# Kernel tuning notes

Hardware: AMD Instinct MI355X
Metric: run time of the kernel (lower is better)

Reference implementation:

```python
import jax, jax.numpy as jnp
import numpy as np

N_NODES = 50000
N_EDGES = 800000
NUM_GRAPHS = 256
F_IN = 64        # num_features (per-head out dim == in dim in this module)
HEADS = 4        # n_heads1
OUT_DIM = 128    # output_dim
HC = HEADS * F_IN
NEG_SLOPE = 0.2  # GATConv leaky_relu slope
EPS = 1e-5       # GraphNorm eps


def setup_inputs() -> dict:
    key = jax.random.key(0)
    ks = jax.random.split(key, 12)
    s = lambda k, shape, fan: (jax.random.normal(k, shape, jnp.float32) / np.sqrt(fan).astype(np.float32))
    return {
        "x": jax.random.normal(ks[0], (N_NODES, F_IN), jnp.float32),
        "edge_index": jax.random.randint(ks[1], (2, N_EDGES), 0, N_NODES),
        "batch": jnp.sort(jax.random.randint(ks[2], (N_NODES,), 0, NUM_GRAPHS)),
        # GATConv params
        "lin_w": s(ks[3], (HC, F_IN), F_IN),
        "att_src": s(ks[4], (HEADS, F_IN), F_IN),
        "att_dst": s(ks[5], (HEADS, F_IN), F_IN),
        "gat_bias": jnp.zeros((HC,), jnp.float32),
        # GraphNorm params
        "gn_weight": jnp.ones((HC,), jnp.float32),
        "gn_bias": jnp.zeros((HC,), jnp.float32),
        "gn_mean_scale": jnp.ones((HC,), jnp.float32),
        # fc_g1 / out heads
        "fc1_w": s(ks[6], (OUT_DIM, HC), HC), "fc1_b": jnp.zeros((OUT_DIM,), jnp.float32),
        "out_w": s(ks[7], (1, OUT_DIM), OUT_DIM), "out_b": jnp.zeros((1,), jnp.float32),
        # GlobalAttention gate_nn: Linear(HC,16) -> ReLU -> Linear(16,1) -> Sigmoid
        "att1_w": s(ks[8], (16, HC), HC), "att1_b": jnp.zeros((16,), jnp.float32),
        "att2_w": s(ks[9], (1, 16), 16), "att2_b": jnp.zeros((1,), jnp.float32),
    }


def _gat_conv(x, edge_index, lin_w, att_src, att_dst, gat_bias):
    """PyG GATConv with add_self_loops=True, concat heads. Returns (out [N,HC], alpha [E+N,H])."""
    N = x.shape[0]
    xh = (x @ lin_w.T).reshape(N, HEADS, F_IN)                 # [N,H,C]
    a_src = (xh * att_src[None]).sum(-1)                        # [N,H]
    a_dst = (xh * att_dst[None]).sum(-1)                        # [N,H]
    loops = jnp.arange(N)
    src = jnp.concatenate([edge_index[0], loops])               # [E+N]
    dst = jnp.concatenate([edge_index[1], loops])
    alpha = jax.nn.leaky_relu(a_src[src] + a_dst[dst], NEG_SLOPE)  # [E+N,H]
    # segment softmax over incoming edges of each dst node (self-loops guarantee non-empty)
    amax = jax.ops.segment_max(alpha, dst, num_segments=N)
    alpha = jnp.exp(alpha - amax[dst])
    denom = jax.ops.segment_sum(alpha, dst, num_segments=N)
    alpha = alpha / (denom[dst] + 1e-16)
    msg = xh[src] * alpha[:, :, None]                           # [E+N,H,C]
    out = jax.ops.segment_sum(msg, dst, num_segments=N).reshape(N, HC) + gat_bias
    return out, alpha


def _graph_norm(x, batch, weight, bias, mean_scale):
    ones = jnp.ones((x.shape[0],), x.dtype)
    cnt = jnp.maximum(jax.ops.segment_sum(ones, batch, num_segments=NUM_GRAPHS), 1.0)[:, None]
    mean = jax.ops.segment_sum(x, batch, num_segments=NUM_GRAPHS) / cnt
    sub = x - mean[batch] * mean_scale
    var = jax.ops.segment_sum(sub * sub, batch, num_segments=NUM_GRAPHS) / cnt
    return weight * sub / jnp.sqrt(var + EPS)[batch] + bias


def _global_attention(x, batch, att1_w, att1_b, att2_w, att2_b):
    gate = jax.nn.sigmoid(jax.nn.relu(x @ att1_w.T + att1_b) @ att2_w.T + att2_b)  # [N,1]
    gmax = jax.ops.segment_max(gate, batch, num_segments=NUM_GRAPHS)
    gate = jnp.exp(gate - gmax[batch])
    gden = jax.ops.segment_sum(gate, batch, num_segments=NUM_GRAPHS)
    gate = gate / (gden[batch] + 1e-16)
    return jax.ops.segment_sum(gate * x, batch, num_segments=NUM_GRAPHS)  # [G,HC]


def reference(x, edge_index, batch, lin_w, att_src, att_dst, gat_bias,
              gn_weight, gn_bias, gn_mean_scale, fc1_w, fc1_b, out_w, out_b,
              att1_w, att1_b, att2_w, att2_b):
    x2, alpha = _gat_conv(x, edge_index, lin_w, att_src, att_dst, gat_bias)
    h = _graph_norm(x2, batch, gn_weight, gn_bias, gn_mean_scale)
    h = jax.nn.relu(h)                                # node_dropout = identity (eval)
    pooled = _global_attention(h, batch, att1_w, att1_b, att2_w, att2_b)
    h = jax.nn.relu(pooled @ fc1_w.T + fc1_b)          # dropout = identity (eval)
    out = jax.nn.sigmoid(h @ out_w.T + out_b)          # [G,1]
    return out, alpha
```

## Files before the change

### kernel.cpp

```cpp
#include <hip/hip_runtime.h>
#include <hip/hip_fp16.h>
#include <math.h>

#define NN 50000
#define NE 800000
#define NG 256
#define NEG_SLOPE 0.2f
#define GEPS 1e-5f
#define NB 196
#define CAP 6144
#define EPB 3125
#define SPLIT 8
#define NLINB 782
#define ABLK 3321

typedef _Float16 f16x8 __attribute__((ext_vector_type(8)));
typedef _Float16 f16x4 __attribute__((ext_vector_type(4)));
typedef float f32x4 __attribute__((ext_vector_type(4)));
typedef float f32x2 __attribute__((ext_vector_type(2)));

__device__ __forceinline__ float lrelu(float v){ return v > 0.f ? v : NEG_SLOPE * v; }

__global__ __launch_bounds__(256) void k_misc(const float* __restrict__ lin_w,
                                              _Float16* __restrict__ wh,
                                              const float* __restrict__ att1_w,
                                              _Float16* __restrict__ a1w,
                                              const int* __restrict__ batch,
                                              int* __restrict__ goff,
                                              int* __restrict__ gcnt,
                                              int* __restrict__ bucket_cnt) {
  int b = blockIdx.x, tid = threadIdx.x;
  if (b == 0) {
    if (tid < NB) bucket_cnt[tid] = 0;
    int g = tid;
    int lo = 0, hi = NN;
    while (lo < hi) { int mid = (lo + hi) >> 1; if (batch[mid] < g) lo = mid + 1; else hi = mid; }
    int start = lo;
    lo = 0; hi = NN;
    while (lo < hi) { int mid = (lo + hi) >> 1; if (batch[mid] < g + 1) lo = mid + 1; else hi = mid; }
    goff[g] = start;
    gcnt[g] = lo - start;
  } else if (b <= 16) {
    int i0 = (b - 1) * 1024 + tid * 4;
    float4 f = *(const float4*)&lin_w[i0];
    f16x4 h4;
    h4[0] = (_Float16)f.x; h4[1] = (_Float16)f.y; h4[2] = (_Float16)f.z; h4[3] = (_Float16)f.w;
    *(f16x4*)&wh[i0] = h4;
  } else {
    int i0 = (b - 17) * 1024 + tid * 4;
    float4 f = *(const float4*)&att1_w[i0];
    f16x4 h4;
    h4[0] = (_Float16)f.x; h4[1] = (_Float16)f.y; h4[2] = (_Float16)f.z; h4[3] = (_Float16)f.w;
    *(f16x4*)&a1w[i0] = h4;
  }
}

__device__ __forceinline__ void lin_body(char* smem,
                                         const float* __restrict__ x,
                                         const _Float16* __restrict__ wh,
                                         const float* __restrict__ att_src,
                                         const float* __restrict__ att_dst,
                                         unsigned char* __restrict__ xh8,
                                         float* __restrict__ a_src_n,
                                         float* __restrict__ a_dst_n) {
  unsigned char* s_f8 = (unsigned char*)smem;
  int w = threadIdx.x >> 6, lane = threadIdx.x & 63;
  int nb = blockIdx.x * 64 + w * 16;
  if (nb >= NN) return;
  int am = lane & 15, quad = lane >> 4;
  int wb = w * 4096;

  const float* xr = x + (size_t)(nb + am) * 64 + quad * 8;
  float4 f0 = *(const float4*)(xr);
  float4 f1 = *(const float4*)(xr + 4);
  float4 f2 = *(const float4*)(xr + 32);
  float4 f3 = *(const float4*)(xr + 36);
  f16x8 a0, a1;
  a0[0] = (_Float16)f0.x; a0[1] = (_Float16)f0.y; a0[2] = (_Float16)f0.z; a0[3] = (_Float16)f0.w;
  a0[4] = (_Float16)f1.x; a0[5] = (_Float16)f1.y; a0[6] = (_Float16)f1.z; a0[7] = (_Float16)f1.w;
  a1[0] = (_Float16)f2.x; a1[1] = (_Float16)f2.y; a1[2] = (_Float16)f2.z; a1[3] = (_Float16)f2.w;
  a1[4] = (_Float16)f3.x; a1[5] = (_Float16)f3.y; a1[6] = (_Float16)f3.z; a1[7] = (_Float16)f3.w;

  f32x4 acc[16];
#pragma unroll
  for (int ct = 0; ct < 16; ct++) acc[ct] = (f32x4){0.f, 0.f, 0.f, 0.f};

#pragma unroll
  for (int ct = 0; ct < 16; ct++) {
    const _Float16* wbp = wh + (size_t)(ct * 16 + am) * 64 + quad * 8;
    f16x8 b0 = *(const f16x8*)(wbp);
    f16x8 b1 = *(const f16x8*)(wbp + 32);
    acc[ct] = __builtin_amdgcn_mfma_f32_16x16x32_f16(a0, b0, acc[ct], 0, 0, 0);
    acc[ct] = __builtin_amdgcn_mfma_f32_16x16x32_f16(a1, b1, acc[ct], 0, 0, 0);
  }

  float ps[4][4], pd[4][4];
#pragma unroll
  for (int r = 0; r < 4; r++)
#pragma unroll
    for (int h = 0; h < 4; h++) { ps[r][h] = 0.f; pd[r][h] = 0.f; }
#pragma unroll
  for (int ct = 0; ct < 16; ct++) {
    int c = ct * 16 + am;
    float av = att_src[c];
    float dv = att_dst[c];
    int h = ct >> 2;
#pragma unroll
    for (int r = 0; r < 4; r++) {
      float v = acc[ct][r];
      ps[r][h] += v * av;
      pd[r][h] += v * dv;
    }
  }
#pragma unroll
  for (int r = 0; r < 4; r++)
#pragma unroll
    for (int h = 0; h < 4; h++) {
      float s = ps[r][h], d = pd[r][h];
#pragma unroll
      for (int o = 1; o < 16; o <<= 1) {
        s += __shfl_xor(s, o, 64);
        d += __shfl_xor(d, o, 64);
      }
      if (am == 0) {
        int node = nb + quad * 4 + r;
        a_src_n[node * 4 + h] = s;
        a_dst_n[node * 4 + h] = d;
      }
    }

#pragma unroll
  for (int r = 0; r < 4; r++) {
    uint4 u;
    int t;
    t = __builtin_amdgcn_cvt_pk_fp8_f32(acc[0][r],  acc[1][r],  0, 0);
    t = __builtin_amdgcn_cvt_pk_fp8_f32(acc[2][r],  acc[3][r],  t, 1);
    u.x = (unsigned)t;
    t = __builtin_amdgcn_cvt_pk_fp8_f32(acc[4][r],  acc[5][r],  0, 0);
    t = __builtin_amdgcn_cvt_pk_fp8_f32(acc[6][r],  acc[7][r],  t, 1);
    u.y = (unsigned)t;
    t = __builtin_amdgcn_cvt_pk_fp8_f32(acc[8][r],  acc[9][r],  0, 0);
    t = __builtin_amdgcn_cvt_pk_fp8_f32(acc[10][r], acc[11][r], t, 1);
    u.z = (unsigned)t;
    t = __builtin_amdgcn_cvt_pk_fp8_f32(acc[12][r], acc[13][r], 0, 0);
    t = __builtin_amdgcn_cvt_pk_fp8_f32(acc[14][r], acc[15][r], t, 1);
    u.w = (unsigned)t;
    *(uint4*)&s_f8[wb + (quad * 4 + r) * 256 + am * 16] = u;
  }
#pragma unroll
  for (int p = 0; p < 4; p++) {
    uint4 u = *(const uint4*)&s_f8[wb + p * 1024 + lane * 16];
    *(uint4*)&xh8[(size_t)nb * 256 + p * 1024 + lane * 16] = u;
  }
}

__device__ __forceinline__ void binA_body(char* smem, int b,
                                          const int* __restrict__ ei,
                                          int* __restrict__ bucket_cnt,
                                          int2* __restrict__ ebuf) {
  int2* sorted = (int2*)smem;
  int*  hist   = (int*)(smem + 25024);
  int*  lbase  = (int*)(smem + 25824);
  int*  cur    = (int*)(smem + 26624);
  int*  runb   = (int*)(smem + 27424);
  int*  wsum   = (int*)(smem + 28224);
  int tid = threadIdx.x, lane = tid & 63, wid = tid >> 6;
  int e0 = b * EPB, e1 = min(e0 + EPB, NE);
  int n = e1 - e0;
  for (int i = tid; i < NB; i += 256) hist[i] = 0;
  __syncthreads();
  for (int e = e0 + tid; e < e1; e += 256) atomicAdd(&hist[ei[NE + e] >> 8], 1);
  __syncthreads();
  {
    int v = (tid < NB) ? hist[tid] : 0;
    int s = v;
#pragma unroll
    for (int o = 1; o < 64; o <<= 1) { int t = __shfl_up(s, o, 64); if (lane >= o) s += t; }
    if (lane == 63) wsum[wid] = s;
    __syncthreads();
    int wbase = 0;
    for (int k = 0; k < wid; k++) wbase += wsum[k];
    if (tid < NB) {
      int ex = wbase + s - v;
      lbase[tid] = ex;
      cur[tid] = ex;
      runb[tid] = atomicAdd(&bucket_cnt[tid], v);
    }
  }
  __syncthreads();
  for (int e = e0 + tid; e < e1; e += 256) {
    int d = ei[NE + e], s = ei[e];
    int lp = atomicAdd(&cur[d >> 8], 1);
    sorted[lp] = make_int2(d, s);
  }
  __syncthreads();
  for (int i = tid; i < n; i += 256) {
    int2 e = sorted[i];
    int bk = e.x >> 8;
    int slot = runb[bk] + (i - lbase[bk]);
    if (slot < CAP) ebuf[(size_t)bk * CAP + slot] = e;
  }
}

__global__ __launch_bounds__(256) void k_linbin(const float* __restrict__ x,
                                                const _Float16* __restrict__ wh,
                                                const float* __restrict__ att_src,
                                                const float* __restrict__ att_dst,
                                                unsigned char* __restrict__ xh8,
                                                float* __restrict__ a_src_n,
                                                float* __restrict__ a_dst_n,
                                                const int* __restrict__ ei,
                                                int* __restrict__ bucket_cnt,
                                                int2* __restrict__ ebuf) {
  __shared__ __align__(16) char smem[28240];
  if (blockIdx.x < NLINB)
    lin_body(smem, x, wh, att_src, att_dst, xh8, a_src_n, a_dst_n);
  else
    binA_body(smem, blockIdx.x - NLINB, ei, bucket_cnt, ebuf);
}

__global__ __launch_bounds__(256) void k_binB(const int2* __restrict__ ebuf,
                                              const int* __restrict__ bucket_cnt,
                                              int* __restrict__ deg,
                                              int* __restrict__ offs,
                                              int* __restrict__ src_list) {
  __shared__ int hist[256];
  __shared__ int cur[256];
  __shared__ int wsum[4];
  __shared__ int bbase[NB];
  int b = blockIdx.x, tid = threadIdx.x, lane = tid & 63, wid = tid >> 6;
  {
    int v = (tid < NB) ? min(bucket_cnt[tid], CAP) : 0;
    int s = v;
#pragma unroll
    for (int o = 1; o < 64; o <<= 1) { int t = __shfl_up(s, o, 64); if (lane >= o) s += t; }
    if (lane == 63) wsum[wid] = s;
    __syncthreads();
    int wbase = 0;
    for (int k = 0; k < wid; k++) wbase += wsum[k];
    if (tid < NB) bbase[tid] = wbase + s - v;
  }
  __syncthreads();
  int cnt = min(bucket_cnt[b], CAP);
  int base = bbase[b];
  const int2* seg = ebuf + (size_t)b * CAP;
  hist[tid] = 0;
  __syncthreads();
  for (int i = tid; i < cnt; i += 256) atomicAdd(&hist[seg[i].x & 255], 1);
  __syncthreads();
  int v = hist[tid];
  int s = v;
#pragma unroll
  for (int o = 1; o < 64; o <<= 1) { int t = __shfl_up(s, o, 64); if (lane >= o) s += t; }
  if (lane == 63) wsum[wid] = s;
  __syncthreads();
  int wbase = 0;
  for (int k = 0; k < wid; k++) wbase += wsum[k];
  int excl = wbase + s - v;
  int node = b * 256 + tid;
  if (node < NN) {
    deg[node] = v;
    offs[node] = base + excl;
  }
  cur[tid] = excl;
  __syncthreads();
  for (int i = tid; i < cnt; i += 256) {
    int2 e = seg[i];
    int pos = base + atomicAdd(&cur[e.x & 255], 1);
    src_list[pos] = e.y;
  }
}

__global__ __launch_bounds__(64) void k_gat(const unsigned char* __restrict__ xh8,
                                            const float* __restrict__ a_src_n,
                                            const float* __restrict__ a_dst_n,
                                            const int* __restrict__ offs,
                                            const int* __restrict__ deg_arr,
                                            const int* __restrict__ src_list,
                                            const float* __restrict__ gat_bias,
                                            __half* __restrict__ x2h,
                                            float* __restrict__ den_inv) {
  __shared__ __align__(16) float s_al[64 * 4];
  __shared__ int s_src[64];
  __shared__ __half s_tr[256];
  int n = blockIdx.x, lane = threadIdx.x;
  int off = offs[n], dg = deg_arr[n], cnt = dg + 1;
  float4 ad = *(const float4*)&a_dst_n[n * 4];
  int am = lane & 15, eg = lane >> 4;
  unsigned loff = (unsigned)am * 16u;

  f32x4 acc[4];
#pragma unroll
  for (int w = 0; w < 4; w++) acc[w] = (f32x4){0.f, 0.f, 0.f, 0.f};
  float s0 = 0.f, s1 = 0.f, s2 = 0.f, s3 = 0.f;

  for (int cb = 0; cb < cnt; cb += 64) {
    int clen = min(64, cnt - cb);
    int pad = (clen + 3) & ~3;
    if (lane < clen) {
      int j = cb + lane;
      int src = (j < dg) ? src_list[off + j] : n;
      float4 as = *(const float4*)&a_src_n[src * 4];
      float e0 = __expf(lrelu(as.x + ad.x));
      float e1 = __expf(lrelu(as.y + ad.y));
      float e2 = __expf(lrelu(as.z + ad.z));
      float e3 = __expf(lrelu(as.w + ad.w));
      s_src[lane] = src;
      *(float4*)&s_al[lane * 4] = make_float4(e0, e1, e2, e3);
      s0 += e0; s1 += e1; s2 += e2; s3 += e3;
    } else if (lane < pad) {
      s_src[lane] = n;
      *(float4*)&s_al[lane * 4] = make_float4(0.f, 0.f, 0.f, 0.f);
    }
    __syncthreads();
    for (int j = 0; j < pad; j += 4) {
      int e = j + eg;
      unsigned oA = ((unsigned)s_src[e] << 8) + loff;
      uint4 r = *(const uint4*)&xh8[oA];
      float4 a4 = *(const float4*)&s_al[e * 4];
      f32x2 l0 = __builtin_amdgcn_cvt_pk_f32_fp8((int)r.x, 0);
      f32x2 h0 = __builtin_amdgcn_cvt_pk_f32_fp8((int)r.x, 1);
      f32x2 l1 = __builtin_amdgcn_cvt_pk_f32_fp8((int)r.y, 0);
      f32x2 h1 = __builtin_amdgcn_cvt_pk_f32_fp8((int)r.y, 1);
      f32x2 l2 = __builtin_amdgcn_cvt_pk_f32_fp8((int)r.z, 0);
      f32x2 h2 = __builtin_amdgcn_cvt_pk_f32_fp8((int)r.z, 1);
      f32x2 l3 = __builtin_amdgcn_cvt_pk_f32_fp8((int)r.w, 0);
      f32x2 h3 = __builtin_amdgcn_cvt_pk_f32_fp8((int)r.w, 1);
      acc[0][0] += a4.x * l0[0]; acc[0][1] += a4.x * l0[1];
      acc[0][2] += a4.x * h0[0]; acc[0][3] += a4.x * h0[1];
      acc[1][0] += a4.y * l1[0]; acc[1][1] += a4.y * l1[1];
      acc[1][2] += a4.y * h1[0]; acc[1][3] += a4.y * h1[1];
      acc[2][0] += a4.z * l2[0]; acc[2][1] += a4.z * l2[1];
      acc[2][2] += a4.z * h2[0]; acc[2][3] += a4.z * h2[1];
      acc[3][0] += a4.w * l3[0]; acc[3][1] += a4.w * l3[1];
      acc[3][2] += a4.w * h3[0]; acc[3][3] += a4.w * h3[1];
    }
    __syncthreads();
  }

#pragma unroll
  for (int o = 32; o >= 1; o >>= 1) {
    s0 += __shfl_xor(s0, o, 64);
    s1 += __shfl_xor(s1, o, 64);
    s2 += __shfl_xor(s2, o, 64);
    s3 += __shfl_xor(s3, o, 64);
  }
  float i0 = 1.f / (s0 + 1e-16f), i1 = 1.f / (s1 + 1e-16f);
  float i2 = 1.f / (s2 + 1e-16f), i3 = 1.f / (s3 + 1e-16f);
  if (lane == 0) *(float4*)&den_inv[n * 4] = make_float4(i0, i1, i2, i3);

#pragma unroll
  for (int w = 0; w < 4; w++)
#pragma unroll
    for (int k = 0; k < 4; k++) {
      float v = acc[w][k];
      v += __shfl_xor(v, 16, 64);
      v += __shfl_xor(v, 32, 64);
      acc[w][k] = v;
    }

  float ivw = (eg == 0) ? i0 : (eg == 1) ? i1 : (eg == 2) ? i2 : i3;
#pragma unroll
  for (int k = 0; k < 4; k++) {
    int c = (4 * eg + k) * 16 + am;
    s_tr[c] = __float2half(acc[eg][k] * ivw + gat_bias[c]);
  }
  __syncthreads();
  uint2 u = *(const uint2*)&s_tr[4 * lane];
  *(uint2*)&x2h[(size_t)n * 256 + 4 * lane] = u;
}

__global__ __launch_bounds__(256) void k_alst(const int* __restrict__ ei,
                                              const float* __restrict__ a_src_n,
                                              const float* __restrict__ a_dst_n,
                                              const float* __restrict__ den_inv,
                                              float* __restrict__ alpha_out,
                                              const __half* __restrict__ x2h,
                                              const int* __restrict__ gcnt,
                                              const int* __restrict__ goff,
                                              float* __restrict__ psumA,
                                              float* __restrict__ psumB) {
  if (blockIdx.x < ABLK) {
    int idx = blockIdx.x * 256 + threadIdx.x;
    if (idx >= NE + NN) return;
    int s, d;
    if (idx < NE) { s = ei[idx]; d = ei[NE + idx]; }
    else          { s = idx - NE; d = s; }
    float4 as = *(const float4*)&a_src_n[s * 4];
    float4 ad = *(const float4*)&a_dst_n[d * 4];
    float4 iv = *(const float4*)&den_inv[d * 4];
    float4 a;
    a.x = __expf(lrelu(as.x + ad.x)) * iv.x;
    a.y = __expf(lrelu(as.y + ad.y)) * iv.y;
    a.z = __expf(lrelu(as.z + ad.z)) * iv.z;
    a.w = __expf(lrelu(as.w + ad.w)) * iv.w;
    *(float4*)&alpha_out[(size_t)idx * 4] = a;
  } else {
    int b = blockIdx.x - ABLK, c = threadIdx.x;
    int g = b >> 3, s = b & 7;
    int cnt = gcnt[g], start = goff[g];
    const __half* p = x2h + (size_t)start * 256 + c;
    float sum = 0.f, sum2 = 0.f;
    int i = s;
    for (; i + 56 < cnt; i += 64) {
      float v0 = __half2float(p[(size_t)(i +  0) * 256]);
      float v1 = __half2float(p[(size_t)(i +  8) * 256]);
      float v2 = __half2float(p[(size_t)(i + 16) * 256]);
      float v3 = __half2float(p[(size_t)(i + 24) * 256]);
      float v4 = __half2float(p[(size_t)(i + 32) * 256]);
      float v5 = __half2float(p[(size_t)(i + 40) * 256]);
      float v6 = __half2float(p[(size_t)(i + 48) * 256]);
      float v7 = __half2float(p[(size_t)(i + 56) * 256]);
      sum += ((v0 + v1) + (v2 + v3)) + ((v4 + v5) + (v6 + v7));
      sum2 += ((v0 * v0 + v1 * v1) + (v2 * v2 + v3 * v3)) +
              ((v4 * v4 + v5 * v5) + (v6 * v6 + v7 * v7));
    }
    for (; i < cnt; i += 8) { float v = __half2float(p[(size_t)i * 256]); sum += v; sum2 += v * v; }
    psumA[b * 256 + c] = sum;
    psumB[b * 256 + c] = sum2;
  }
}

__global__ __launch_bounds__(256) void k_stats2(const float* __restrict__ psumA,
                                                const float* __restrict__ psumB,
                                                const int* __restrict__ gcnt,
                                                const float* __restrict__ gn_w,
                                                const float* __restrict__ gn_b,
                                                const float* __restrict__ gn_ms,
                                                float* __restrict__ scale_g,
                                                float* __restrict__ shift_g) {
  int g = blockIdx.x, c = threadIdx.x;
  int b0 = g * SPLIT;
  float S = 0.f, S2 = 0.f;
#pragma unroll
  for (int k = 0; k < SPLIT; k++) {
    S  += psumA[(b0 + k) * 256 + c];
    S2 += psumB[(b0 + k) * 256 + c];
  }
  float fc = fmaxf((float)gcnt[g], 1.f);
  float mean = S / fc;
  float mm = mean * gn_ms[c];
  float var = fmaxf(S2 / fc - 2.f * mm * mean + mm * mm, 0.f);
  float sc = gn_w[c] / sqrtf(var + GEPS);
  scale_g[g * 256 + c] = sc;
  shift_g[g * 256 + c] = gn_b[c] - sc * mm;
}

__global__ __launch_bounds__(256) void k_gate(const __half* __restrict__ x2h,
                                              const int* __restrict__ batch,
                                              const float* __restrict__ scale_g,
                                              const float* __restrict__ shift_g,
                                              const _Float16* __restrict__ a1w,
                                              const float* __restrict__ att1_b,
                                              const float* __restrict__ att2_w,
                                              const float* __restrict__ att2_b,
                                              float* __restrict__ gate_raw) {
  int w = threadIdx.x >> 6, lane = threadIdx.x & 63;
  int nb = blockIdx.x * 64 + w * 16;
  if (nb >= NN) return;
  int am = lane & 15, quad = lane >> 4;
  int node = nb + am;
  int g = batch[node];

  const __half*   xp  = x2h + (size_t)node * 256 + quad * 8;
  const float*    scp = scale_g + g * 256 + quad * 8;
  const float*    shp = shift_g + g * 256 + quad * 8;
  const _Float16* bp  = a1w + am * 256 + quad * 8;

  f32x4 acc = (f32x4){0.f, 0.f, 0.f, 0.f};
#pragma unroll
  for (int kb = 0; kb < 8; kb++) {
    f16x8 xv = *(const f16x8*)(xp + kb * 32);
    float4 sc0 = *(const float4*)(scp + kb * 32);
    float4 sc1 = *(const float4*)(scp + kb * 32 + 4);
    float4 sh0 = *(const float4*)(shp + kb * 32);
    float4 sh1 = *(const float4*)(shp + kb * 32 + 4);
    f16x8 a;
    a[0] = (_Float16)fmaxf(sc0.x * (float)xv[0] + sh0.x, 0.f);
    a[1] = (_Float16)fmaxf(sc0.y * (float)xv[1] + sh0.y, 0.f);
    a[2] = (_Float16)fmaxf(sc0.z * (float)xv[2] + sh0.z, 0.f);
    a[3] = (_Float16)fmaxf(sc0.w * (float)xv[3] + sh0.w, 0.f);
    a[4] = (_Float16)fmaxf(sc1.x * (float)xv[4] + sh1.x, 0.f);
    a[5] = (_Float16)fmaxf(sc1.y * (float)xv[5] + sh1.y, 0.f);
    a[6] = (_Float16)fmaxf(sc1.z * (float)xv[6] + sh1.z, 0.f);
    a[7] = (_Float16)fmaxf(sc1.w * (float)xv[7] + sh1.w, 0.f);
    f16x8 b = *(const f16x8*)(bp + kb * 32);
    acc = __builtin_amdgcn_mfma_f32_16x16x32_f16(a, b, acc, 0, 0, 0);
  }

  float b1 = att1_b[am], w2 = att2_w[am], b2 = att2_b[0];
#pragma unroll
  for (int r = 0; r < 4; r++) {
    float t = w2 * fmaxf(acc[r] + b1, 0.f);
#pragma unroll
    for (int o = 1; o < 16; o <<= 1) t += __shfl_xor(t, o, 64);
    if (am == 0) gate_raw[nb + quad * 4 + r] = 1.f / (1.f + __expf(-(t + b2)));
  }
}

__global__ __launch_bounds__(256) void k_poolp(const __half* __restrict__ x2h,
                                               const float* __restrict__ gate_raw,
                                               const int* __restrict__ gcnt,
                                               const int* __restrict__ goff,
                                               const float* __restrict__ scale_g,
                                               const float* __restrict__ shift_g,
                                               float* __restrict__ ppool) {
  __shared__ float s_w[1024];
  __shared__ float red[4];
  int b = blockIdx.x, c = threadIdx.x, lane = c & 63, wid = c >> 6;
  int g = b >> 3, s = b & 7;
  int cnt = gcnt[g], start = goff[g];
  float ls = 0.f;
  for (int i = c; i < cnt; i += 256) {
    float e = __expf(gate_raw[start + i]);
    s_w[i] = e;
    ls += e;
  }
#pragma unroll
  for (int o = 32; o >= 1; o >>= 1) ls += __shfl_xor(ls, o, 64);
  if (lane == 0) red[wid] = ls;
  __syncthreads();
  float rden = 1.f / (red[0] + red[1] + red[2] + red[3] + 1e-16f);

  float sc = scale_g[g * 256 + c], sh = shift_g[g * 256 + c];
  const __half* p = x2h + (size_t)start * 256 + c;
  float pooled = 0.f;
  int i = s;
  for (; i + 56 < cnt; i += 64) {
    float v0 = __half2float(p[(size_t)(i +  0) * 256]);
    float v1 = __half2float(p[(size_t)(i +  8) * 256]);
    float v2 = __half2float(p[(size_t)(i + 16) * 256]);
    float v3 = __half2float(p[(size_t)(i + 24) * 256]);
    float v4 = __half2float(p[(size_t)(i + 32) * 256]);
    float v5 = __half2float(p[(size_t)(i + 40) * 256]);
    float v6 = __half2float(p[(size_t)(i + 48) * 256]);
    float v7 = __half2float(p[(size_t)(i + 56) * 256]);
    pooled += s_w[i +  0] * fmaxf(sc * v0 + sh, 0.f);
    pooled += s_w[i +  8] * fmaxf(sc * v1 + sh, 0.f);
    pooled += s_w[i + 16] * fmaxf(sc * v2 + sh, 0.f);
    pooled += s_w[i + 24] * fmaxf(sc * v3 + sh, 0.f);
    pooled += s_w[i + 32] * fmaxf(sc * v4 + sh, 0.f);
    pooled += s_w[i + 40] * fmaxf(sc * v5 + sh, 0.f);
    pooled += s_w[i + 48] * fmaxf(sc * v6 + sh, 0.f);
    pooled += s_w[i + 56] * fmaxf(sc * v7 + sh, 0.f);
  }
  for (; i < cnt; i += 8)
    pooled += s_w[i] * fmaxf(sc * __half2float(p[(size_t)i * 256]) + sh, 0.f);
  ppool[b * 256 + c] = pooled * rden;
}

__global__ __launch_bounds__(256) void k_fin(const float* __restrict__ ppool,
                                             const float* __restrict__ fc1_w,
                                             const float* __restrict__ fc1_b,
                                             const float* __restrict__ out_w,
                                             const float* __restrict__ out_b,
                                             float* __restrict__ outp) {
  __shared__ __align__(16) float pool_s[256];
  __shared__ float hred[128];
  __shared__ float red[4];
  int g = blockIdx.x, tid = threadIdx.x, lane = tid & 63, wid = tid >> 6;
  int b0 = g * SPLIT;
  float acc = 0.f;
#pragma unroll
  for (int k = 0; k < SPLIT; k++) acc += ppool[(b0 + k) * 256 + tid];
  pool_s[tid] = acc;
  __syncthreads();
  float4 psv = *(const float4*)&pool_s[4 * lane];
  for (int j0 = 0; j0 < 32; j0++) {
    int j = wid * 32 + j0;
    float4 w = *(const float4*)&fc1_w[j * 256 + 4 * lane];
    float d = w.x * psv.x + w.y * psv.y + w.z * psv.z + w.w * psv.w;
#pragma unroll
    for (int o = 32; o >= 1; o >>= 1) d += __shfl_xor(d, o, 64);
    if (lane == 0) hred[j] = fmaxf(d + fc1_b[j], 0.f) * out_w[j];
  }
  __syncthreads();
  if (tid < 128) {
    float v = hred[tid];
#pragma unroll
    for (int o = 32; o >= 1; o >>= 1) v += __shfl_xor(v, o, 64);
    if (lane == 0) red[wid] = v;
  }
  __syncthreads();
  if (tid == 0) outp[g] = 1.f / (1.f + __expf(-(red[0] + red[1] + out_b[0])));
}

extern "C" void kernel_launch(void* const* d_in, const int* in_sizes, int n_in,
                              void* d_out, int out_size, void* d_ws, size_t ws_size,
                              hipStream_t stream) {
  const float* x        = (const float*)d_in[0];
  const int*   ei       = (const int*)d_in[1];
  const int*   batch    = (const int*)d_in[2];
  const float* lin_w    = (const float*)d_in[3];
  const float* att_src  = (const float*)d_in[4];
  const float* att_dst  = (const float*)d_in[5];
  const float* gat_bias = (const float*)d_in[6];
  const float* gn_w     = (const float*)d_in[7];
  const float* gn_b     = (const float*)d_in[8];
  const float* gn_ms    = (const float*)d_in[9];
  const float* fc1_w    = (const float*)d_in[10];
  const float* fc1_b    = (const float*)d_in[11];
  const float* out_w    = (const float*)d_in[12];
  const float* out_b    = (const float*)d_in[13];
  const float* att1_w   = (const float*)d_in[14];
  const float* att1_b   = (const float*)d_in[15];
  const float* att2_w   = (const float*)d_in[16];
  const float* att2_b   = (const float*)d_in[17];

  float* outp  = (float*)d_out;
  float* alpha = outp + NG;

  char* wsb = (char*)d_ws;
  size_t o = 0;
  auto A = [&](size_t bytes) -> char* {
    char* p = wsb + o;
    o += (bytes + 255) & ~(size_t)255;
    return p;
  };
  unsigned char* xh8 = (unsigned char*)A((size_t)NN * 256);
  __half*   x2h      = (__half*)A((size_t)NN * 256 * 2);
  _Float16* wh       = (_Float16*)A((size_t)256 * 64 * 2);
  _Float16* a1w      = (_Float16*)A((size_t)16 * 256 * 2);
  float* a_src_n  = (float*)A((size_t)NN * 4 * 4);
  float* a_dst_n  = (float*)A((size_t)NN * 4 * 4);
  float* den_inv  = (float*)A((size_t)NN * 4 * 4);
  float* gate_raw = (float*)A((size_t)NN * 4);
  float* psumA    = (float*)A((size_t)NG * SPLIT * 256 * 4);
  float* psumB    = (float*)A((size_t)NG * SPLIT * 256 * 4);
  float* ppool    = (float*)A((size_t)NG * SPLIT * 256 * 4);
  float* scale_g  = (float*)A((size_t)NG * 256 * 4);
  float* shift_g  = (float*)A((size_t)NG * 256 * 4);
  int*   deg      = (int*)A((size_t)NN * 4);
  int*   gcnt     = (int*)A((size_t)NG * 4);
  int*   offs     = (int*)A((size_t)NN * 4);
  int*   goff     = (int*)A((size_t)NG * 4);
  int*   src_list = (int*)A((size_t)NE * 4);
  int2*  ebuf     = (int2*)A((size_t)NB * CAP * 8);
  int*   bucket_cnt  = (int*)A((size_t)NB * 4);

  k_misc<<<21, 256, 0, stream>>>(lin_w, wh, att1_w, a1w, batch, goff, gcnt, bucket_cnt);
  k_linbin<<<NLINB + 256, 256, 0, stream>>>(x, wh, att_src, att_dst, xh8, a_src_n, a_dst_n,
                                            ei, bucket_cnt, ebuf);
  k_binB<<<NB, 256, 0, stream>>>(ebuf, bucket_cnt, deg, offs, src_list);
  k_gat<<<NN, 64, 0, stream>>>(xh8, a_src_n, a_dst_n, offs, deg, src_list,
                               gat_bias, x2h, den_inv);
  k_alst<<<ABLK + NG * SPLIT, 256, 0, stream>>>(ei, a_src_n, a_dst_n, den_inv, alpha,
                                                x2h, gcnt, goff, psumA, psumB);
  k_stats2<<<NG, 256, 0, stream>>>(psumA, psumB, gcnt, gn_w, gn_b, gn_ms, scale_g, shift_g);
  k_gate<<<(NN + 63) / 64, 256, 0, stream>>>(x2h, batch, scale_g, shift_g, a1w, att1_b,
                                             att2_w, att2_b, gate_raw);
  k_poolp<<<NG * SPLIT, 256, 0, stream>>>(x2h, gate_raw, gcnt, goff, scale_g, shift_g, ppool);
  k_fin<<<NG, 256, 0, stream>>>(ppool, fc1_w, fc1_b, out_w, out_b, outp);
}
```

Before: 266.4 us.

## Pack four nodes per block in GAT aggregation with per-lane channel ownership

The GAT neighbour-aggregation kernel now runs four destination nodes per 256-thread block, one wavefront each, instead of one 64-thread block per node. Each lane owns four fp8 channels and walks every edge, unrolled by four, rather than splitting edges into four groups that need cross-lane shuffle reductions. This removes the block-wide barriers, the padding of edge chunks and the final reduction, and it gives coalesced 256-byte row reads per edge. In exchange each lane issues more narrow 4-byte loads, and the code relies on wavefront-synchronous shared-memory ordering with no explicit barrier.

```diff
diff --git a/kernel.cpp b/kernel.cpp
--- a/kernel.cpp
+++ b/kernel.cpp
@@ -271,32 +271,30 @@
   }
 }
 
-__global__ __launch_bounds__(64) void k_gat(const unsigned char* __restrict__ xh8,
-                                            const float* __restrict__ a_src_n,
-                                            const float* __restrict__ a_dst_n,
-                                            const int* __restrict__ offs,
-                                            const int* __restrict__ deg_arr,
-                                            const int* __restrict__ src_list,
-                                            const float* __restrict__ gat_bias,
-                                            __half* __restrict__ x2h,
-                                            float* __restrict__ den_inv) {
-  __shared__ __align__(16) float s_al[64 * 4];
-  __shared__ int s_src[64];
-  __shared__ __half s_tr[256];
-  int n = blockIdx.x, lane = threadIdx.x;
+__global__ __launch_bounds__(256) void k_gat(const unsigned char* __restrict__ xh8,
+                                             const float* __restrict__ a_src_n,
+                                             const float* __restrict__ a_dst_n,
+                                             const int* __restrict__ offs,
+                                             const int* __restrict__ deg_arr,
+                                             const int* __restrict__ src_list,
+                                             const float* __restrict__ gat_bias,
+                                             __half* __restrict__ x2h,
+                                             float* __restrict__ den_inv) {
+  __shared__ __align__(16) float s_al[4][64 * 4];
+  __shared__ int s_src[4][64];
+  __shared__ __half s_tr[4][256];
+  int w = threadIdx.x >> 6, lane = threadIdx.x & 63;
+  int n = blockIdx.x * 4 + w;
   int off = offs[n], dg = deg_arr[n], cnt = dg + 1;
   float4 ad = *(const float4*)&a_dst_n[n * 4];
-  int am = lane & 15, eg = lane >> 4;
-  unsigned loff = (unsigned)am * 16u;
-
-  f32x4 acc[4];
-#pragma unroll
-  for (int w = 0; w < 4; w++) acc[w] = (f32x4){0.f, 0.f, 0.f, 0.f};
+  int h = lane & 3;
+  unsigned loff = 4u * (unsigned)lane;
+
+  float acc0 = 0.f, acc1 = 0.f, acc2 = 0.f, acc3 = 0.f;
   float s0 = 0.f, s1 = 0.f, s2 = 0.f, s3 = 0.f;
 
   for (int cb = 0; cb < cnt; cb += 64) {
     int clen = min(64, cnt - cb);
-    int pad = (clen + 3) & ~3;
     if (lane < clen) {
       int j = cb + lane;
       int src = (j < dg) ? src_list[off + j] : n;
@@ -305,37 +303,46 @@
       float e1 = __expf(lrelu(as.y + ad.y));
       float e2 = __expf(lrelu(as.z + ad.z));
       float e3 = __expf(lrelu(as.w + ad.w));
-      s_src[lane] = src;
-      *(float4*)&s_al[lane * 4] = make_float4(e0, e1, e2, e3);
+      s_src[w][lane] = src;
+      *(float4*)&s_al[w][lane * 4] = make_float4(e0, e1, e2, e3);
       s0 += e0; s1 += e1; s2 += e2; s3 += e3;
-    } else if (lane < pad) {
-      s_src[lane] = n;
-      *(float4*)&s_al[lane * 4] = make_float4(0.f, 0.f, 0.f, 0.f);
     }
-    __syncthreads();
-    for (int j = 0; j < pad; j += 4) {
-      int e = j + eg;
-      unsigned oA = ((unsigned)s_src[e] << 8) + loff;
-      uint4 r = *(const uint4*)&xh8[oA];
-      float4 a4 = *(const float4*)&s_al[e * 4];
-      f32x2 l0 = __builtin_amdgcn_cvt_pk_f32_fp8((int)r.x, 0);
-      f32x2 h0 = __builtin_amdgcn_cvt_pk_f32_fp8((int)r.x, 1);
-      f32x2 l1 = __builtin_amdgcn_cvt_pk_f32_fp8((int)r.y, 0);
-      f32x2 h1 = __builtin_amdgcn_cvt_pk_f32_fp8((int)r.y, 1);
-      f32x2 l2 = __builtin_amdgcn_cvt_pk_f32_fp8((int)r.z, 0);
-      f32x2 h2 = __builtin_amdgcn_cvt_pk_f32_fp8((int)r.z, 1);
-      f32x2 l3 = __builtin_amdgcn_cvt_pk_f32_fp8((int)r.w, 0);
-      f32x2 h3 = __builtin_amdgcn_cvt_pk_f32_fp8((int)r.w, 1);
-      acc[0][0] += a4.x * l0[0]; acc[0][1] += a4.x * l0[1];
-      acc[0][2] += a4.x * h0[0]; acc[0][3] += a4.x * h0[1];
-      acc[1][0] += a4.y * l1[0]; acc[1][1] += a4.y * l1[1];
-      acc[1][2] += a4.y * h1[0]; acc[1][3] += a4.y * h1[1];
-      acc[2][0] += a4.z * l2[0]; acc[2][1] += a4.z * l2[1];
-      acc[2][2] += a4.z * h2[0]; acc[2][3] += a4.z * h2[1];
-      acc[3][0] += a4.w * l3[0]; acc[3][1] += a4.w * l3[1];
-      acc[3][2] += a4.w * h3[0]; acc[3][3] += a4.w * h3[1];
+    int j = 0;
+    for (; j + 4 <= clen; j += 4) {
+      unsigned oA = ((unsigned)s_src[w][j]     << 8) + loff;
+      unsigned oB = ((unsigned)s_src[w][j + 1] << 8) + loff;
+      unsigned oC = ((unsigned)s_src[w][j + 2] << 8) + loff;
+      unsigned oD = ((unsigned)s_src[w][j + 3] << 8) + loff;
+      unsigned rA = *(const unsigned*)&xh8[oA];
+      unsigned rB = *(const unsigned*)&xh8[oB];
+      unsigned rC = *(const unsigned*)&xh8[oC];
+      unsigned rD = *(const unsigned*)&xh8[oD];
+      float aA = s_al[w][j * 4 + h],       aB = s_al[w][(j + 1) * 4 + h];
+      float aC = s_al[w][(j + 2) * 4 + h], aD = s_al[w][(j + 3) * 4 + h];
+      f32x2 lA = __builtin_amdgcn_cvt_pk_f32_fp8((int)rA, 0);
+      f32x2 hA = __builtin_amdgcn_cvt_pk_f32_fp8((int)rA, 1);
+      f32x2 lB = __builtin_amdgcn_cvt_pk_f32_fp8((int)rB, 0);
+      f32x2 hB = __builtin_amdgcn_cvt_pk_f32_fp8((int)rB, 1);
+      f32x2 lC = __builtin_amdgcn_cvt_pk_f32_fp8((int)rC, 0);
+      f32x2 hC = __builtin_amdgcn_cvt_pk_f32_fp8((int)rC, 1);
+      f32x2 lD = __builtin_amdgcn_cvt_pk_f32_fp8((int)rD, 0);
+      f32x2 hD = __builtin_amdgcn_cvt_pk_f32_fp8((int)rD, 1);
+      acc0 += aA * lA[0] + aB * lB[0] + aC * lC[0] + aD * lD[0];
+      acc1 += aA * lA[1] + aB * lB[1] + aC * lC[1] + aD * lD[1];
+      acc2 += aA * hA[0] + aB * hB[0] + aC * hC[0] + aD * hD[0];
+      acc3 += aA * hA[1] + aB * hB[1] + aC * hC[1] + aD * hD[1];
     }
-    __syncthreads();
+    for (; j < clen; j++) {
+      unsigned oA = ((unsigned)s_src[w][j] << 8) + loff;
+      unsigned rA = *(const unsigned*)&xh8[oA];
+      float aA = s_al[w][j * 4 + h];
+      f32x2 lA = __builtin_amdgcn_cvt_pk_f32_fp8((int)rA, 0);
+      f32x2 hA = __builtin_amdgcn_cvt_pk_f32_fp8((int)rA, 1);
+      acc0 += aA * lA[0];
+      acc1 += aA * lA[1];
+      acc2 += aA * hA[0];
+      acc3 += aA * hA[1];
+    }
   }
 
 #pragma unroll
@@ -349,24 +356,13 @@
   float i2 = 1.f / (s2 + 1e-16f), i3 = 1.f / (s3 + 1e-16f);
   if (lane == 0) *(float4*)&den_inv[n * 4] = make_float4(i0, i1, i2, i3);
 
-#pragma unroll
-  for (int w = 0; w < 4; w++)
-#pragma unroll
-    for (int k = 0; k < 4; k++) {
-      float v = acc[w][k];
-      v += __shfl_xor(v, 16, 64);
-      v += __shfl_xor(v, 32, 64);
-      acc[w][k] = v;
-    }
-
-  float ivw = (eg == 0) ? i0 : (eg == 1) ? i1 : (eg == 2) ? i2 : i3;
-#pragma unroll
-  for (int k = 0; k < 4; k++) {
-    int c = (4 * eg + k) * 16 + am;
-    s_tr[c] = __float2half(acc[eg][k] * ivw + gat_bias[c]);
-  }
-  __syncthreads();
-  uint2 u = *(const uint2*)&s_tr[4 * lane];
+  float ivh = (h == 0) ? i0 : (h == 1) ? i1 : (h == 2) ? i2 : i3;
+  int cb0 = (lane & 3) * 64 + (lane >> 2);
+  s_tr[w][cb0 +  0] = __float2half(acc0 * ivh + gat_bias[cb0 +  0]);
+  s_tr[w][cb0 + 16] = __float2half(acc1 * ivh + gat_bias[cb0 + 16]);
+  s_tr[w][cb0 + 32] = __float2half(acc2 * ivh + gat_bias[cb0 + 32]);
+  s_tr[w][cb0 + 48] = __float2half(acc3 * ivh + gat_bias[cb0 + 48]);
+  uint2 u = *(const uint2*)&s_tr[w][4 * lane];
   *(uint2*)&x2h[(size_t)n * 256 + 4 * lane] = u;
 }
 
@@ -642,8 +638,8 @@
   k_linbin<<<NLINB + 256, 256, 0, stream>>>(x, wh, att_src, att_dst, xh8, a_src_n, a_dst_n,
                                             ei, bucket_cnt, ebuf);
   k_binB<<<NB, 256, 0, stream>>>(ebuf, bucket_cnt, deg, offs, src_list);
-  k_gat<<<NN, 64, 0, stream>>>(xh8, a_src_n, a_dst_n, offs, deg, src_list,
-                               gat_bias, x2h, den_inv);
+  k_gat<<<NN / 4, 256, 0, stream>>>(xh8, a_src_n, a_dst_n, offs, deg, src_list,
+                                    gat_bias, x2h, den_inv);
   k_alst<<<ABLK + NG * SPLIT, 256, 0, stream>>>(ei, a_src_n, a_dst_n, den_inv, alpha,
                                                 x2h, gcnt, goff, psumA, psumB);
   k_stats2<<<NG, 256, 0, stream>>>(psumA, psumB, gcnt, gn_w, gn_b, gn_ms, scale_g, shift_g);
```

After: 254.7 us. 4.4% less time.
